# Kernel tuning notes

Measured on AMD Instinct MI355X. Metric: run time of the kernel, lower is better.

Reference implementation:

```python
import jax, jax.numpy as jnp
import numpy as np

B, H, W, C = 64, 14, 14, 768

def setup_inputs() -> dict:
    key = jax.random.key(0)
    k = jax.random.split(key, 5)
    s = 0.02  # small init so tanh/sigmoid stay in active range
    return {
        "x": jax.random.normal(k[0], (B, H, W, C), dtype=jnp.float32),
        "Wx": jax.random.normal(k[1], (3 * C, C), dtype=jnp.float32) * s,
        "bx": jnp.zeros((3 * C,), dtype=jnp.float32),
        "Wh": jax.random.normal(k[2], (3 * C, C), dtype=jnp.float32) * s,
        "bh": jnp.zeros((3 * C,), dtype=jnp.float32),
        "Wp": jax.random.normal(k[3], (C, C), dtype=jnp.float32) * s,
    }

def reference(x, Wx, bx, Wh, bh, Wp):
    b, h_, w_, c = x.shape
    n = h_ * w_
    seq = x.reshape(b, n, c)
    # Input projections for all timesteps at once (no recurrent dependency).
    x_zrn = jnp.einsum('bnc,dc->bnd', seq, Wx) + bx  # [B, N, 3C]
    x_zrn_t = jnp.transpose(x_zrn, (1, 0, 2))        # [N, B, 3C] for scan

    def step(h, xz):
        h_zrn = h @ Wh.T + bh                         # [B, 3C]
        x_z, x_r, x_n = jnp.split(xz, 3, axis=-1)
        h_z, h_r, h_n = jnp.split(h_zrn, 3, axis=-1)
        z = jax.nn.sigmoid(x_z + h_z)
        r = jax.nn.sigmoid(x_r + h_r)
        ncand = jnp.tanh(x_n + r * h_n)
        h_new = (1.0 - z) * ncand + z * h
        return h_new, h_new

    h0 = jnp.zeros((b, c), dtype=x.dtype)
    _, hs = jax.lax.scan(step, h0, x_zrn_t)           # hs: [N, B, C]
    y = jnp.transpose(hs, (1, 0, 2))                  # [B, N, C]
    y = jnp.einsum('bnc,dc->bnd', y, Wp)              # proj (no bias)
    # proj_drop = 0.0 -> identity
    return y.reshape(b, h_, w_, c)
```

## Files before the change

### kernel.cpp

```cpp
#include <hip/hip_runtime.h>

typedef unsigned short u16;
typedef unsigned int   u32;
typedef unsigned long long u64;
typedef __attribute__((ext_vector_type(8))) short bf16x8;
typedef __attribute__((ext_vector_type(4))) float f32x4;

#define GK 768
#define NSTEP 196
#define NWG 96
#define CPW 8
#define RROWS 24
#define HSTEP 49152

__device__ __forceinline__ u16 f2bf(float f) {
    u32 u = __float_as_uint(f);
    u = (u + 0x7fffu + ((u >> 16) & 1u)) >> 16;
    return (u16)u;
}
__device__ __forceinline__ float bf2f(u16 h) { return __uint_as_float(((u32)h) << 16); }

__global__ __launch_bounds__(256) void cvt_kernel(
    const float4* __restrict__ x, const float4* __restrict__ wx,
    const float4* __restrict__ wp,
    u32* __restrict__ xb, u32* __restrict__ wxb, u32* __restrict__ wpb,
    int* __restrict__ flags)
{
    const int N1 = 9633792 / 4, N2 = 1769472 / 4;
    int i = blockIdx.x * 256 + threadIdx.x;
    if (blockIdx.x == 0) flags[threadIdx.x] = 0;
    const float4* src; u32* dst; int off;
    if (i < N1)            { src = x;  dst = xb;  off = i; }
    else if (i < N1 + N2)  { src = wx; dst = wxb; off = i - N1; }
    else                   { src = wp; dst = wpb; off = i - N1 - N2; }
    float4 v = src[off];
    u32 lo = (u32)f2bf(v.x) | ((u32)f2bf(v.y) << 16);
    u32 hi = (u32)f2bf(v.z) | ((u32)f2bf(v.w) << 16);
    dst[(size_t)off * 2]     = lo;
    dst[(size_t)off * 2 + 1] = hi;
}

template<int MODE>
__global__ __launch_bounds__(256) void gemm_bt(
    const u16* __restrict__ A, const u16* __restrict__ B,
    const float* __restrict__ bias, void* __restrict__ outv)
{
    __shared__ u16 As[128 * 40];
    __shared__ u16 Bs[128 * 40];
    const int tid  = threadIdx.x;
    const int lane = tid & 63;
    const int wv   = tid >> 6;
    const int m0 = blockIdx.y * 128;
    const int n0 = blockIdx.x * 128;
    const int wm = (wv & 1) * 64;
    const int wn = (wv >> 1) * 64;

    f32x4 acc[4][4];
#pragma unroll
    for (int i = 0; i < 4; ++i)
#pragma unroll
        for (int j = 0; j < 4; ++j) acc[i][j] = (f32x4){0.f, 0.f, 0.f, 0.f};

    const int r0 = tid >> 2, q0 = tid & 3;
    const u16* gA0 = A + (size_t)(m0 + r0)      * GK + q0 * 8;
    const u16* gA1 = A + (size_t)(m0 + r0 + 64) * GK + q0 * 8;
    const u16* gB0 = B + (size_t)(n0 + r0)      * GK + q0 * 8;
    const u16* gB1 = B + (size_t)(n0 + r0 + 64) * GK + q0 * 8;
    u16* sA0 = As + r0 * 40 + q0 * 8;
    u16* sA1 = As + (r0 + 64) * 40 + q0 * 8;
    u16* sB0 = Bs + r0 * 40 + q0 * 8;
    u16* sB1 = Bs + (r0 + 64) * 40 + q0 * 8;

    const int fr = lane & 15, fq = lane >> 4;
    const u16* fA = As + (wm + fr) * 40 + fq * 8;
    const u16* fB = Bs + (wn + fr) * 40 + fq * 8;

    for (int kt = 0; kt < GK / 32; ++kt) {
        uint4 a0 = *(const uint4*)(gA0 + kt * 32);
        uint4 a1 = *(const uint4*)(gA1 + kt * 32);
        uint4 b0 = *(const uint4*)(gB0 + kt * 32);
        uint4 b1 = *(const uint4*)(gB1 + kt * 32);
        __syncthreads();
        *(uint4*)sA0 = a0; *(uint4*)sA1 = a1;
        *(uint4*)sB0 = b0; *(uint4*)sB1 = b1;
        __syncthreads();
        bf16x8 af[4], bfr[4];
#pragma unroll
        for (int mi = 0; mi < 4; ++mi) af[mi]  = *(const bf16x8*)(fA + mi * 16 * 40);
#pragma unroll
        for (int ni = 0; ni < 4; ++ni) bfr[ni] = *(const bf16x8*)(fB + ni * 16 * 40);
#pragma unroll
        for (int mi = 0; mi < 4; ++mi)
#pragma unroll
            for (int ni = 0; ni < 4; ++ni)
                acc[mi][ni] = __builtin_amdgcn_mfma_f32_16x16x32_bf16(
                    af[mi], bfr[ni], acc[mi][ni], 0, 0, 0);
    }

    if (MODE == 1) {
        u16* out = (u16*)outv;
#pragma unroll
        for (int mi = 0; mi < 4; ++mi) {
#pragma unroll
            for (int ni = 0; ni < 4; ++ni) {
                int col = n0 + wn + ni * 16 + fr;
                float bv = bias[col];
#pragma unroll
                for (int r = 0; r < 4; ++r) {
                    int m = m0 + wm + mi * 16 + fq * 4 + r;
                    int b = m / 196;
                    int nn = m - b * 196;
                    u16 hv = f2bf(acc[mi][ni][r] + bv);
                    int other = __shfl_xor((int)hv, 1, 64);
                    if (!(lane & 1)) {
                        u32 packed = (u32)hv | (((u32)(u16)other) << 16);
                        size_t eidx = ((size_t)nn * 64 + (size_t)b) * 2304 + (size_t)col;
                        *((u32*)out + (eidx >> 1)) = packed;
                    }
                }
            }
        }
    } else {
        float* out = (float*)outv;
#pragma unroll
        for (int mi = 0; mi < 4; ++mi) {
#pragma unroll
            for (int ni = 0; ni < 4; ++ni) {
                int col = n0 + wn + ni * 16 + fr;
#pragma unroll
                for (int r = 0; r < 4; ++r) {
                    int m = m0 + wm + mi * 16 + fq * 4 + r;
                    int b = m & 63;
                    int nn = m >> 6;
                    out[((size_t)b * 196 + nn) * 768 + col] = acc[mi][ni][r];
                }
            }
        }
    }
}

__global__ __launch_bounds__(512) void recur_kernel(
    const u16* __restrict__ xz,
    const float* __restrict__ Wh,
    const float* __restrict__ bh,
    u16* __restrict__ hsx,
    int* flags)
{
    __shared__ float hz_s[2][64 * 28];
    __shared__ float hold_s[512];

    const int tid  = threadIdx.x;
    const int wg   = blockIdx.x;
    const int c0   = wg * CPW;
    const int lane = tid & 63;
    const int wv   = tid >> 6;
    const int mi   = wv & 3;
    const int kh   = wv >> 2;
    const int fr   = lane & 15, fq = lane >> 4;

    __builtin_amdgcn_fence(__ATOMIC_ACQUIRE, "agent");

    bf16x8 bfrag[2][12];
#pragma unroll
    for (int ni = 0; ni < 2; ++ni) {
        int row = ni * 16 + fr;
        bool valid = row < RROWS;
        int gate = row >> 3, ch = row & 7;
        const float* wp = Wh + (size_t)(valid ? (gate * 768 + c0 + ch) : 0) * 768;
#pragma unroll
        for (int kk = 0; kk < 12; ++kk) {
            int k0 = (kh * 12 + kk) * 32 + fq * 8;
            float4 f0 = *(const float4*)(wp + k0);
            float4 f1 = *(const float4*)(wp + k0 + 4);
            bf16x8 b;
            b[0] = (short)f2bf(f0.x); b[1] = (short)f2bf(f0.y);
            b[2] = (short)f2bf(f0.z); b[3] = (short)f2bf(f0.w);
            b[4] = (short)f2bf(f1.x); b[5] = (short)f2bf(f1.y);
            b[6] = (short)f2bf(f1.z); b[7] = (short)f2bf(f1.w);
            if (!valid) b = (bf16x8){0,0,0,0,0,0,0,0};
            bfrag[ni][kk] = b;
        }
    }

    hold_s[tid] = 0.f;
    __syncthreads();

    const int gb = tid >> 3, gi = tid & 7;
    const int gc = c0 + gi;
    const float bh0 = bh[gc], bh1 = bh[768 + gc], bh2 = bh[1536 + gc];

    const int aoff = (mi * 16 + fr) * 768 + kh * 384 + fq * 8;

    for (int n = 0; n < NSTEP; ++n) {
        size_t xoff = (size_t)n * 147456 + (size_t)gb * 2304 + (size_t)gc;
        float xg0 = bf2f(xz[xoff]);
        float xg1 = bf2f(xz[xoff + 768]);
        float xg2 = bf2f(xz[xoff + 1536]);

        f32x4 acc0 = (f32x4){0.f, 0.f, 0.f, 0.f};
        f32x4 acc1 = (f32x4){0.f, 0.f, 0.f, 0.f};

        if (n > 0) {
            for (;;) {
                int v0 = __hip_atomic_load(&flags[lane], __ATOMIC_RELAXED,
                                           __HIP_MEMORY_SCOPE_AGENT);
                int v1 = __hip_atomic_load(&flags[lane + 32], __ATOMIC_RELAXED,
                                           __HIP_MEMORY_SCOPE_AGENT);
                if (__all((v0 < v1 ? v0 : v1) >= n)) break;
            }

            const u16* ap = hsx + (size_t)(n - 1) * HSTEP + aoff;
#pragma unroll
            for (int kk = 0; kk < 12; ++kk) {
                bf16x8 a = *(const bf16x8*)(ap + kk * 32);
                acc0 = __builtin_amdgcn_mfma_f32_16x16x32_bf16(a, bfrag[0][kk], acc0, 0, 0, 0);
                acc1 = __builtin_amdgcn_mfma_f32_16x16x32_bf16(a, bfrag[1][kk], acc1, 0, 0, 0);
            }
        }

        {
            int bat = mi * 16 + fq * 4;
#pragma unroll
            for (int r = 0; r < 4; ++r)
                hz_s[kh][(bat + r) * 28 + fr] = acc0[r];
            if (fr < 8) {
#pragma unroll
                for (int r = 0; r < 4; ++r)
                    hz_s[kh][(bat + r) * 28 + 16 + fr] = acc1[r];
            }
        }
        __syncthreads();

        float h0 = hz_s[0][gb * 28 + gi]      + hz_s[1][gb * 28 + gi]      + bh0;
        float h1 = hz_s[0][gb * 28 + 8 + gi]  + hz_s[1][gb * 28 + 8 + gi]  + bh1;
        float h2 = hz_s[0][gb * 28 + 16 + gi] + hz_s[1][gb * 28 + 16 + gi] + bh2;
        float z  = 1.f / (1.f + __expf(-(xg0 + h0)));
        float rr = 1.f / (1.f + __expf(-(xg1 + h1)));
        float pre = xg2 + rr * h2;
        float e2 = __expf(-2.f * pre);
        float nc = (1.f - e2) / (1.f + e2);
        float hold = hold_s[tid];
        float hnew = (1.f - z) * nc + z * hold;
        hold_s[tid] = hnew;

        u16 hv = f2bf(hnew);
        u32 other = ((u32)__shfl_xor((int)hv, 1, 64)) & 0xffffu;
        u32 v01 = (u32)hv | (other << 16);
        u32 v23 = (u32)__shfl_xor((int)v01, 2, 64);
        if ((tid & 3) == 0) {
            u64 q = (u64)v01 | ((u64)v23 << 32);
            size_t ofs = (size_t)n * HSTEP + (size_t)gb * 768 + (size_t)gc;
            __hip_atomic_store((u64*)((u32*)hsx + (ofs >> 1)), q,
                               __ATOMIC_RELAXED, __HIP_MEMORY_SCOPE_AGENT);
        }
        __syncthreads();
        if (tid == 0)
            __hip_atomic_store(&flags[wg], n + 1, __ATOMIC_RELAXED,
                               __HIP_MEMORY_SCOPE_AGENT);
    }
}

extern "C" void kernel_launch(void* const* d_in, const int* in_sizes, int n_in,
                              void* d_out, int out_size, void* d_ws, size_t ws_size,
                              hipStream_t stream)
{
    const float* x  = (const float*)d_in[0];
    const float* Wx = (const float*)d_in[1];
    const float* bx = (const float*)d_in[2];
    const float* Wh = (const float*)d_in[3];
    const float* bh = (const float*)d_in[4];
    const float* Wp = (const float*)d_in[5];
    float* out = (float*)d_out;

    char* ws = (char*)d_ws;
    size_t off = 0;
    auto wsalloc = [&](size_t bytes) -> void* {
        void* p = ws + off;
        off += (bytes + 255) & ~(size_t)255;
        return p;
    };
    u16* xb   = (u16*)wsalloc(9633792ull * 2);
    u16* wxb  = (u16*)wsalloc(1769472ull * 2);
    u16* wpb  = (u16*)wsalloc(589824ull * 2);
    u16* xzrn = (u16*)wsalloc(196ull * 64 * 2304 * 2);
    u16* hsx  = (u16*)wsalloc(196ull * 64 * 768 * 2);
    int* flags = (int*)wsalloc(1024);

    cvt_kernel<<<11712, 256, 0, stream>>>(
        (const float4*)x, (const float4*)Wx, (const float4*)Wp,
        (u32*)xb, (u32*)wxb, (u32*)wpb, flags);

    gemm_bt<1><<<dim3(18, 98), 256, 0, stream>>>(xb, wxb, bx, (void*)xzrn);

    {
        const u16* a0 = xzrn; const float* a1 = Wh; const float* a2 = bh;
        u16* a3 = hsx; int* a4 = flags;
        void* args[5] = { &a0, &a1, &a2, &a3, &a4 };
        hipLaunchCooperativeKernel((void*)recur_kernel, dim3(NWG), dim3(512),
                                   args, 0, stream);
    }

    gemm_bt<0><<<dim3(6, 98), 256, 0, stream>>>(hsx, wpb, nullptr, (void*)out);
}
```

Before: 1.348 ms.

## Partition GRU recurrence by batch per XCC with L2-local flag polling

The recurrent kernel is restructured so each XCC (read via HW_REG_XCC_ID) owns 8 batch rows, and 24 workgroups per XCC each handle 32 channels across all three gates. Because each batch group is independent, step synchronisation then only spans workgroups on the same XCC. Those workgroups can poll flags with buffer_inv plus a plain load from the local L2 and publish with plain stores, avoiding agent-scope coherence traffic across XCCs. A mirror flag and a timeout fall back to atomic polling. If blocks are not spread evenly over XCCs, the kernel uses a non-local path with agent-scope atomics. The cost is that half of each MFMA tile is padding (8 of 16 rows), and correctness depends on XCC placement and cache-coherence assumptions.

Result: slower. 1.496 ms (+11.0%).

```diff
diff --git a/kernel.cpp b/kernel.cpp
--- a/kernel.cpp
+++ b/kernel.cpp
@@ -8,10 +8,11 @@
 
 #define GK 768
 #define NSTEP 196
-#define NWG 96
-#define CPW 8
-#define RROWS 24
 #define HSTEP 49152
+#define PWG 24
+#define NBLK 256
+#define FLAG0 32
+#define MIR0 512
 
 __device__ __forceinline__ u16 f2bf(float f) {
     u32 u = __float_as_uint(f);
@@ -28,7 +29,12 @@
 {
     const int N1 = 9633792 / 4, N2 = 1769472 / 4;
     int i = blockIdx.x * 256 + threadIdx.x;
-    if (blockIdx.x == 0) flags[threadIdx.x] = 0;
+    if (blockIdx.x == 0) {
+        flags[threadIdx.x]       = 0;
+        flags[256 + threadIdx.x] = 0;
+        flags[512 + threadIdx.x] = 0;
+        flags[768 + threadIdx.x] = 0;
+    }
     const float4* src; u32* dst; int off;
     if (i < N1)            { src = x;  dst = xb;  off = i; }
     else if (i < N1 + N2)  { src = wx; dst = wxb; off = i - N1; }
@@ -139,124 +145,198 @@
     }
 }
 
-__global__ __launch_bounds__(512) void recur_kernel(
-    const u16* __restrict__ xz,
-    const float* __restrict__ Wh,
-    const float* __restrict__ bh,
-    u16* __restrict__ hsx,
-    int* flags)
-{
-    __shared__ float hz_s[2][64 * 28];
-    __shared__ float hold_s[512];
-
-    const int tid  = threadIdx.x;
-    const int wg   = blockIdx.x;
-    const int c0   = wg * CPW;
+__device__ __forceinline__ int poll_load_l2(const int* p) {
+    int v;
+    asm volatile("buffer_inv\n\t"
+                 "global_load_dword %0, %1, off\n\t"
+                 "s_waitcnt vmcnt(0)"
+                 : "=v"(v) : "v"(p) : "memory");
+    return v;
+}
+__device__ __forceinline__ void store_plain(int* p, int v) {
+    asm volatile("global_store_dword %0, %1, off"
+                 :: "v"(p), "v"(v) : "memory");
+}
+
+template<bool LOCAL>
+__device__ void recur_run(
+    int g, int s, int tid,
+    const u16* __restrict__ xz, const float* __restrict__ Wh,
+    const float* __restrict__ bh, u16* __restrict__ hsx, int* flags,
+    float* hzs)
+{
     const int lane = tid & 63;
     const int wv   = tid >> 6;
-    const int mi   = wv & 3;
-    const int kh   = wv >> 2;
+    const int kh   = wv & 1;
+    const int np   = wv >> 1;
     const int fr   = lane & 15, fq = lane >> 4;
-
-    __builtin_amdgcn_fence(__ATOMIC_ACQUIRE, "agent");
+    const int c0   = s * 32;
+    const int B0   = g * 8;
 
     bf16x8 bfrag[2][12];
 #pragma unroll
-    for (int ni = 0; ni < 2; ++ni) {
-        int row = ni * 16 + fr;
-        bool valid = row < RROWS;
-        int gate = row >> 3, ch = row & 7;
-        const float* wp = Wh + (size_t)(valid ? (gate * 768 + c0 + ch) : 0) * 768;
+    for (int j = 0; j < 2; ++j) {
+        int row = np * 768 + c0 + j * 16 + fr;
+        const float* wp = Wh + (size_t)row * 768 + kh * 384 + fq * 8;
 #pragma unroll
         for (int kk = 0; kk < 12; ++kk) {
-            int k0 = (kh * 12 + kk) * 32 + fq * 8;
-            float4 f0 = *(const float4*)(wp + k0);
-            float4 f1 = *(const float4*)(wp + k0 + 4);
+            float4 f0 = *(const float4*)(wp + kk * 32);
+            float4 f1 = *(const float4*)(wp + kk * 32 + 4);
             bf16x8 b;
             b[0] = (short)f2bf(f0.x); b[1] = (short)f2bf(f0.y);
             b[2] = (short)f2bf(f0.z); b[3] = (short)f2bf(f0.w);
             b[4] = (short)f2bf(f1.x); b[5] = (short)f2bf(f1.y);
             b[6] = (short)f2bf(f1.z); b[7] = (short)f2bf(f1.w);
-            if (!valid) b = (bf16x8){0,0,0,0,0,0,0,0};
-            bfrag[ni][kk] = b;
-        }
-    }
-
-    hold_s[tid] = 0.f;
-    __syncthreads();
-
-    const int gb = tid >> 3, gi = tid & 7;
+            bfrag[j][kk] = b;
+        }
+    }
+
+    const int gb = tid >> 5, gi = tid & 31;
     const int gc = c0 + gi;
-    const float bh0 = bh[gc], bh1 = bh[768 + gc], bh2 = bh[1536 + gc];
-
-    const int aoff = (mi * 16 + fr) * 768 + kh * 384 + fq * 8;
+    float bh0 = 0.f, bh1 = 0.f, bh2 = 0.f, hold = 0.f;
+    if (tid < 256) { bh0 = bh[gc]; bh1 = bh[768 + gc]; bh2 = bh[1536 + gc]; }
+
+    int fl = lane;
+    if (fl >= 48) fl -= 48; else if (fl >= 24) fl -= 24;
+    int* const myflag      = &flags[FLAG0 + g * 32 + s];
+    int* const mymir       = &flags[MIR0  + g * 32 + s];
+    const int* const pollf = &flags[FLAG0 + g * 32 + fl];
+    const int* const pollm = &flags[MIR0  + g * 32 + fl];
+
+    bool slow = !LOCAL;
 
     for (int n = 0; n < NSTEP; ++n) {
-        size_t xoff = (size_t)n * 147456 + (size_t)gb * 2304 + (size_t)gc;
-        float xg0 = bf2f(xz[xoff]);
-        float xg1 = bf2f(xz[xoff + 768]);
-        float xg2 = bf2f(xz[xoff + 1536]);
+        float xg0 = 0.f, xg1 = 0.f, xg2 = 0.f;
+        if (tid < 256) {
+            size_t xoff = ((size_t)n * 64 + (B0 + gb)) * 2304 + gc;
+            xg0 = bf2f(xz[xoff]);
+            xg1 = bf2f(xz[xoff + 768]);
+            xg2 = bf2f(xz[xoff + 1536]);
+        }
 
         f32x4 acc0 = (f32x4){0.f, 0.f, 0.f, 0.f};
         f32x4 acc1 = (f32x4){0.f, 0.f, 0.f, 0.f};
 
         if (n > 0) {
-            for (;;) {
-                int v0 = __hip_atomic_load(&flags[lane], __ATOMIC_RELAXED,
-                                           __HIP_MEMORY_SCOPE_AGENT);
-                int v1 = __hip_atomic_load(&flags[lane + 32], __ATOMIC_RELAXED,
-                                           __HIP_MEMORY_SCOPE_AGENT);
-                if (__all((v0 < v1 ? v0 : v1) >= n)) break;
-            }
-
-            const u16* ap = hsx + (size_t)(n - 1) * HSTEP + aoff;
+            if (!slow) {
+                int tries = 0;
+                for (;;) {
+                    int v = poll_load_l2(pollf);
+                    if (__all(v >= n)) break;
+                    if (++tries > 3000) { slow = true; break; }
+                }
+            }
+            if (slow) {
+                const int* pp = LOCAL ? pollm : pollf;
+                for (;;) {
+                    int v = __hip_atomic_load(pp, __ATOMIC_RELAXED,
+                                              __HIP_MEMORY_SCOPE_AGENT);
+                    if (__all(v >= n)) break;
+                }
+            }
+            const u16* ap = hsx + (size_t)(n - 1) * HSTEP
+                                + (size_t)(B0 + fr) * 768 + kh * 384 + fq * 8;
+            const bool arow = fr < 8;
 #pragma unroll
             for (int kk = 0; kk < 12; ++kk) {
-                bf16x8 a = *(const bf16x8*)(ap + kk * 32);
+                bf16x8 a = arow ? *(const bf16x8*)(ap + kk * 32)
+                                : (bf16x8){0, 0, 0, 0, 0, 0, 0, 0};
                 acc0 = __builtin_amdgcn_mfma_f32_16x16x32_bf16(a, bfrag[0][kk], acc0, 0, 0, 0);
                 acc1 = __builtin_amdgcn_mfma_f32_16x16x32_bf16(a, bfrag[1][kk], acc1, 0, 0, 0);
             }
         }
 
-        {
-            int bat = mi * 16 + fq * 4;
-#pragma unroll
-            for (int r = 0; r < 4; ++r)
-                hz_s[kh][(bat + r) * 28 + fr] = acc0[r];
-            if (fr < 8) {
-#pragma unroll
-                for (int r = 0; r < 4; ++r)
-                    hz_s[kh][(bat + r) * 28 + 16 + fr] = acc1[r];
+#pragma unroll
+        for (int r = 0; r < 4; ++r) {
+            int b = fq * 4 + r;
+            if (b < 8) {
+                hzs[(kh * 8 + b) * 96 + np * 32 + fr]      = acc0[r];
+                hzs[(kh * 8 + b) * 96 + np * 32 + 16 + fr] = acc1[r];
             }
         }
         __syncthreads();
 
-        float h0 = hz_s[0][gb * 28 + gi]      + hz_s[1][gb * 28 + gi]      + bh0;
-        float h1 = hz_s[0][gb * 28 + 8 + gi]  + hz_s[1][gb * 28 + 8 + gi]  + bh1;
-        float h2 = hz_s[0][gb * 28 + 16 + gi] + hz_s[1][gb * 28 + 16 + gi] + bh2;
-        float z  = 1.f / (1.f + __expf(-(xg0 + h0)));
-        float rr = 1.f / (1.f + __expf(-(xg1 + h1)));
-        float pre = xg2 + rr * h2;
-        float e2 = __expf(-2.f * pre);
-        float nc = (1.f - e2) / (1.f + e2);
-        float hold = hold_s[tid];
-        float hnew = (1.f - z) * nc + z * hold;
-        hold_s[tid] = hnew;
-
-        u16 hv = f2bf(hnew);
-        u32 other = ((u32)__shfl_xor((int)hv, 1, 64)) & 0xffffu;
-        u32 v01 = (u32)hv | (other << 16);
-        u32 v23 = (u32)__shfl_xor((int)v01, 2, 64);
-        if ((tid & 3) == 0) {
-            u64 q = (u64)v01 | ((u64)v23 << 32);
-            size_t ofs = (size_t)n * HSTEP + (size_t)gb * 768 + (size_t)gc;
-            __hip_atomic_store((u64*)((u32*)hsx + (ofs >> 1)), q,
-                               __ATOMIC_RELAXED, __HIP_MEMORY_SCOPE_AGENT);
-        }
+        if (tid < 256) {
+            float h0 = hzs[gb * 96 + gi]      + hzs[(8 + gb) * 96 + gi]      + bh0;
+            float h1 = hzs[gb * 96 + 32 + gi] + hzs[(8 + gb) * 96 + 32 + gi] + bh1;
+            float h2 = hzs[gb * 96 + 64 + gi] + hzs[(8 + gb) * 96 + 64 + gi] + bh2;
+            float z   = 1.f / (1.f + __expf(-(xg0 + h0)));
+            float rr2 = 1.f / (1.f + __expf(-(xg1 + h1)));
+            float pre = xg2 + rr2 * h2;
+            float e2  = __expf(-2.f * pre);
+            float nc  = (1.f - e2) / (1.f + e2);
+            float hnew = (1.f - z) * nc + z * hold;
+            hold = hnew;
+
+            u16 hv = f2bf(hnew);
+            u32 other = ((u32)__shfl_xor((int)hv, 1, 64)) & 0xffffu;
+            u32 v01 = (u32)hv | (other << 16);
+            u32 v23 = (u32)__shfl_xor((int)v01, 2, 64);
+            if ((tid & 3) == 0) {
+                u64 q = (u64)v01 | ((u64)v23 << 32);
+                size_t ofs = (size_t)n * HSTEP + (size_t)(B0 + gb) * 768 + gc;
+                u64* p = (u64*)(hsx + ofs);
+                if (LOCAL) {
+                    *p = q;
+                } else {
+                    __hip_atomic_store(p, q, __ATOMIC_RELAXED, __HIP_MEMORY_SCOPE_AGENT);
+                }
+            }
+        }
+        asm volatile("s_waitcnt vmcnt(0)" ::: "memory");
         __syncthreads();
-        if (tid == 0)
-            __hip_atomic_store(&flags[wg], n + 1, __ATOMIC_RELAXED,
+        if (LOCAL) {
+            if (tid == 0)
+                store_plain(myflag, n + 1);
+            else if (tid == 64)
+                __hip_atomic_store(mymir, n + 1, __ATOMIC_RELAXED,
+                                   __HIP_MEMORY_SCOPE_AGENT);
+        } else {
+            if (tid == 0)
+                __hip_atomic_store(myflag, n + 1, __ATOMIC_RELAXED,
+                                   __HIP_MEMORY_SCOPE_AGENT);
+        }
+    }
+}
+
+__global__ __launch_bounds__(384) void recur2_kernel(
+    const u16* __restrict__ xz, const float* __restrict__ Wh,
+    const float* __restrict__ bh, u16* __restrict__ hsx, int* flags)
+{
+    __shared__ float hzs[2 * 8 * 96];
+    __shared__ int sh_g, sh_s;
+    const int tid = threadIdx.x;
+
+    __builtin_amdgcn_fence(__ATOMIC_ACQUIRE, "agent");
+
+    if (tid == 0) {
+        u32 xcc = 0;
+        asm volatile("s_getreg_b32 %0, hwreg(HW_REG_XCC_ID)" : "=s"(xcc));
+        int gg = (int)(xcc & 7u);
+        sh_g = gg;
+        sh_s = __hip_atomic_fetch_add(&flags[gg], 1, __ATOMIC_ACQ_REL,
+                                      __HIP_MEMORY_SCOPE_AGENT);
+        __hip_atomic_fetch_add(&flags[15], 1, __ATOMIC_ACQ_REL,
                                __HIP_MEMORY_SCOPE_AGENT);
+        while (__hip_atomic_load(&flags[15], __ATOMIC_ACQUIRE,
+                                 __HIP_MEMORY_SCOPE_AGENT) < NBLK) {}
+    }
+    __syncthreads();
+    const int g = sh_g, s = sh_s;
+
+    bool ok = true;
+#pragma unroll
+    for (int x = 0; x < 8; ++x)
+        ok &= (__hip_atomic_load(&flags[x], __ATOMIC_RELAXED,
+                                 __HIP_MEMORY_SCOPE_AGENT) >= PWG);
+
+    if (ok) {
+        if (s < PWG)
+            recur_run<true>(g, s, tid, xz, Wh, bh, hsx, flags, hzs);
+    } else {
+        const int bid = blockIdx.x;
+        if (bid < 8 * PWG)
+            recur_run<false>(bid & 7, bid >> 3, tid, xz, Wh, bh, hsx, flags, hzs);
     }
 }
 
@@ -284,7 +364,7 @@
     u16* wpb  = (u16*)wsalloc(589824ull * 2);
     u16* xzrn = (u16*)wsalloc(196ull * 64 * 2304 * 2);
     u16* hsx  = (u16*)wsalloc(196ull * 64 * 768 * 2);
-    int* flags = (int*)wsalloc(1024);
+    int* flags = (int*)wsalloc(4096);
 
     cvt_kernel<<<11712, 256, 0, stream>>>(
         (const float4*)x, (const float4*)Wx, (const float4*)Wp,
@@ -296,7 +376,7 @@
         const u16* a0 = xzrn; const float* a1 = Wh; const float* a2 = bh;
         u16* a3 = hsx; int* a4 = flags;
         void* args[5] = { &a0, &a1, &a2, &a3, &a4 };
-        hipLaunchCooperativeKernel((void*)recur_kernel, dim3(NWG), dim3(512),
+        hipLaunchCooperativeKernel((void*)recur2_kernel, dim3(NBLK), dim3(384),
                                    args, 0, stream);
     }
 
```
